# Kernel optimization log

Hardware: AMD Instinct MI355X
Metric: run time of the kernel (lower is better)

Reference implementation:

```python
import jax, jax.numpy as jnp
import numpy as np
from jax import lax

B, T, N_MELS = 8, 4096, 26
W_FRAMES = 32          # window_frames
CONV_CH, CONV_K = 64, 5
SE_MID = CONV_CH // 4  # se_ratio=4 on feature_dim=conv_channels
H1, H2 = 256, 128      # hidden_dims
SHORT_W, SHORT_H = 8, 128
OUT_CH = 2             # downbeat=True


def setup_inputs() -> dict:
    key = jax.random.key(0)
    ks = jax.random.split(key, 16)
    s = lambda *sh: 1.0 / np.sqrt(sh[0])
    return {
        "x": jax.random.normal(ks[0], (B, T, N_MELS), jnp.float32),
        # conv1d: kernel stored (K, in, out) for NWC/WIO conv
        "conv_w": jax.random.normal(ks[1], (CONV_K, N_MELS, CONV_CH), jnp.float32) * 0.1,
        "conv_b": jax.random.normal(ks[2], (CONV_CH,), jnp.float32) * 0.1,
        # SE on feature_dim=CONV_CH
        "se_w1": jax.random.normal(ks[3], (CONV_CH, SE_MID), jnp.float32) * s(CONV_CH),
        "se_b1": jnp.zeros((SE_MID,), jnp.float32),
        "se_w2": jax.random.normal(ks[4], (SE_MID, CONV_CH), jnp.float32) * s(SE_MID),
        "se_b2": jnp.zeros((CONV_CH,), jnp.float32),
        # long backbone: (W_FRAMES*CONV_CH) -> H1 -> H2
        "w1": jax.random.normal(ks[5], (W_FRAMES * CONV_CH, H1), jnp.float32) * s(W_FRAMES * CONV_CH),
        "b1": jnp.zeros((H1,), jnp.float32),
        "w2": jax.random.normal(ks[6], (H1, H2), jnp.float32) * s(H1),
        "b2": jnp.zeros((H2,), jnp.float32),
        # short backbone: (SHORT_W*CONV_CH) -> SHORT_H
        "sw": jax.random.normal(ks[7], (SHORT_W * CONV_CH, SHORT_H), jnp.float32) * s(SHORT_W * CONV_CH),
        "sb": jnp.zeros((SHORT_H,), jnp.float32),
        # output head: (H2 + SHORT_H) -> OUT_CH
        "wo": jax.random.normal(ks[8], (H2 + SHORT_H, OUT_CH), jnp.float32) * s(H2 + SHORT_H),
        "bo": jnp.zeros((OUT_CH,), jnp.float32),
    }


def reference(x, conv_w, conv_b, se_w1, se_b1, se_w2, se_b2,
              w1, b1, w2, b2, sw, sb, wo, bo):
    batch, time, _ = x.shape
    # 1) causal conv1d over full sequence (left-pad K-1), then ReLU
    xp = jnp.pad(x, ((0, 0), (CONV_K - 1, 0), (0, 0)))
    xc = lax.conv_general_dilated(xp, conv_w, window_strides=(1,),
                                  padding='VALID',
                                  dimension_numbers=('NWC', 'WIO', 'NWC'))
    xc = jax.nn.relu(xc + conv_b)                      # (B, T, F=CONV_CH)
    # 2) causal sliding-window unfold: windows[b,t,w,:] = padded[b, t+w, :]
    x_pad = jnp.pad(xc, ((0, 0), (W_FRAMES - 1, 0), (0, 0)))
    idx = jnp.arange(time)[:, None] + jnp.arange(W_FRAMES)[None, :]
    windows = x_pad[:, idx, :]                          # (B, T, W, F)
    # 3) SE channel attention (pool over window dim)
    s = windows.mean(axis=2)                            # (B, T, F)
    a = jax.nn.sigmoid(jax.nn.relu(s @ se_w1 + se_b1) @ se_w2 + se_b2)
    windows = windows * a[:, :, None, :]
    # 4) long backbone (dropout = identity in eval)
    flat_long = windows.reshape(batch, time, W_FRAMES * CONV_CH)
    h = jax.nn.relu(flat_long @ w1 + b1)
    h = jax.nn.relu(h @ w2 + b2)                        # (B, T, H2)
    # short path: last SHORT_W frames of the same SE-processed window
    flat_short = windows[:, :, -SHORT_W:, :].reshape(batch, time, SHORT_W * CONV_CH)
    h_short = jax.nn.relu(flat_short @ sw + sb)         # (B, T, SHORT_H)
    h = jnp.concatenate([h, h_short], axis=-1)
    # 5) output head
    return jax.nn.sigmoid(h @ wo + bo)                  # (B, T, OUT_CH)
```

## Files before the change

### kernel.cpp

```cpp
#include <hip/hip_runtime.h>

typedef _Float16 half_t;
typedef __attribute__((ext_vector_type(8))) _Float16 h8;
typedef __attribute__((ext_vector_type(2))) _Float16 h2v;
typedef __attribute__((ext_vector_type(4))) float f4;
typedef __attribute__((ext_vector_type(2))) float f2v;

__device__ __forceinline__ half_t to_h(float v) {
    v = fminf(fmaxf(v, -60000.f), 60000.f);
    return (half_t)v;
}

__global__ void pack_k(const float* __restrict__ w1, const float* __restrict__ w2,
                       const float* __restrict__ sw, const float* __restrict__ cw,
                       half_t* __restrict__ wsH) {
    int i = blockIdx.x * 256 + threadIdx.x;
    if (i < 65536) {
        int L = i & 63, nt = (i >> 6) & 15, kk = i >> 10;
        int k0 = kk * 32 + ((L >> 4) << 3), n = (nt << 4) + (L & 15);
        h8 v;
#pragma unroll
        for (int j = 0; j < 8; j++) v[j] = to_h(w1[(k0 + j) * 256 + n]);
        *(h8*)(wsH + ((((kk * 16 + nt) * 64 + L)) << 3)) = v;
    } else if (i < 69632) {
        int o = i - 65536;
        int L = o & 63, nt = (o >> 6) & 7, kk = o >> 9;
        int k0 = kk * 32 + ((L >> 4) << 3), n = (nt << 4) + (L & 15);
        h8 v;
#pragma unroll
        for (int j = 0; j < 8; j++) v[j] = to_h(w2[(k0 + j) * 128 + n]);
        *(h8*)(wsH + 524288 + ((((kk * 8 + nt) * 64 + L)) << 3)) = v;
    } else if (i < 77824) {
        int o = i - 69632;
        int L = o & 63, nt = (o >> 6) & 7, kk = o >> 9;
        int k0 = kk * 32 + ((L >> 4) << 3), n = (nt << 4) + (L & 15);
        h8 v;
#pragma unroll
        for (int j = 0; j < 8; j++) v[j] = to_h(sw[(k0 + j) * 128 + n]);
        *(h8*)(wsH + 557056 + ((((kk * 8 + nt) * 64 + L)) << 3)) = v;
    } else if (i < 86144) {
        int o = i - 77824;
        int c = o & 63, rest = o >> 6;
        int k = rest / 26, ci = rest - k * 26;
        int ip = ci >> 1, r = ci & 1;
        wsH[622592 + ((k * 13 + ip) * 64 + c) * 2 + r] = to_h(cw[o]);
    }
}

#define XCS 72
#define ALS 72
#define Y1S 264
#define SLS 68
#define HLS 20

#define MFMA16(a, b, c) __builtin_amdgcn_mfma_f32_16x16x32_f16(a, b, c, 0, 0, 0)

__global__ __launch_bounds__(512, 4) void beat_main(
    const float* __restrict__ x,
    const float* __restrict__ conv_b,
    const float* __restrict__ se_w1, const float* __restrict__ se_b1,
    const float* __restrict__ se_w2, const float* __restrict__ se_b2,
    const float* __restrict__ b1, const float* __restrict__ b2,
    const float* __restrict__ sb,
    const float* __restrict__ wo, const float* __restrict__ bo,
    const half_t* __restrict__ w1p, const half_t* __restrict__ w2p,
    const half_t* __restrict__ swp, const half_t* __restrict__ cwp,
    float* __restrict__ out) {

    __shared__ __align__(16) char smem[58752];
    half_t* xcL = (half_t*)smem;
    half_t* aL  = (half_t*)(smem + 13696);
    char*   U   = smem + 22912;
    half_t* xLh = (half_t*)U;
    float*  sLf = (float*)U;
    float*  hidL= (float*)(U + 17408);
    half_t* y1L = (half_t*)U;
    float*  woL = (float*)(smem + 56704);

    const int tid = threadIdx.x;
    const int bi = blockIdx.x;
    const int b = bi >> 6;
    const int t0 = (bi & 63) << 6;
    const int lane = tid & 63, wv = tid >> 6;
    const int quad = lane >> 4, rl = lane & 15;

    if (tid < 256) ((f2v*)woL)[tid] = ((const f2v*)wo)[tid];
    for (int idx = tid; idx < 99 * 13; idx += 512) {
        int fi = idx / 13, ip = idx - fi * 13;
        int tx = t0 - 35 + fi;
        h2v v;
        if (tx >= 0) {
            const float* xp = x + ((size_t)(b * 4096 + tx)) * 26 + 2 * ip;
            v[0] = to_h(xp[0]); v[1] = to_h(xp[1]);
        } else { v[0] = (_Float16)0.f; v[1] = (_Float16)0.f; }
        *(h2v*)(xLh + fi * 28 + 2 * ip) = v;
    }
    __syncthreads();

    {
        int c = tid & 63, f0 = tid >> 6;
        h2v cwr[65];
        const h2v* cwg = (const h2v*)cwp;
#pragma unroll
        for (int p = 0; p < 65; p++) cwr[p] = cwg[p * 64 + c];
        float bias = conv_b[c];
        for (int f = f0; f < 95; f += 8) {
            int t = t0 - 31 + f;
            float r0 = 0.f;
            if (t >= 0) {
                h2v accp; accp[0] = (_Float16)0.f; accp[1] = (_Float16)0.f;
#pragma unroll
                for (int k = 0; k < 5; k++)
#pragma unroll
                    for (int ip = 0; ip < 13; ip++) {
                        h2v xp = *(const h2v*)(xLh + (f + k) * 28 + 2 * ip);
                        accp += xp * cwr[k * 13 + ip];
                    }
                r0 = fmaxf((float)accp[0] + (float)accp[1] + bias, 0.f);
            }
            xcL[f * XCS + c] = to_h(r0);
        }
    }
    __syncthreads();

    {
        int c = tid & 63, mb = tid >> 6;
        float run = 0.f;
#pragma unroll 8
        for (int w = 0; w < 32; w++) run += (float)xcL[(mb + w) * XCS + c];
        sLf[mb * SLS + c] = run * (1.f / 32.f);
        for (int m = mb + 8; m < 64; m += 8) {
#pragma unroll
            for (int d = 0; d < 8; d++) {
                run += (float)xcL[(m + 24 + d) * XCS + c];
                run -= (float)xcL[(m - 8 + d) * XCS + c];
            }
            sLf[m * SLS + c] = run * (1.f / 32.f);
        }
    }
    __syncthreads();

    {
        int m = tid >> 3, hh = (tid & 7) * 2;
        float acc0 = se_b1[hh], acc1 = se_b1[hh + 1];
        for (int c = 0; c < 64; c++) {
            float sv = sLf[m * SLS + c];
            f2v wq = *(const f2v*)(se_w1 + c * 16 + hh);
            acc0 += sv * wq[0]; acc1 += sv * wq[1];
        }
        hidL[m * HLS + hh] = fmaxf(acc0, 0.f);
        hidL[m * HLS + hh + 1] = fmaxf(acc1, 0.f);
    }
    __syncthreads();

    {
        int m = tid >> 3, c0 = (tid & 7) * 8;
        float av[8];
#pragma unroll
        for (int j = 0; j < 8; j++) av[j] = se_b2[c0 + j];
        for (int h = 0; h < 16; h++) {
            float hv = hidL[m * HLS + h];
            const f4* wv4 = (const f4*)(se_w2 + h * 64 + c0);
            f4 wq0 = wv4[0], wq1 = wv4[1];
#pragma unroll
            for (int j = 0; j < 4; j++) { av[j] += hv * wq0[j]; av[4 + j] += hv * wq1[j]; }
        }
#pragma unroll
        for (int j = 0; j < 8; j++) {
            float zz = fminf(fmaxf(av[j], -30.f), 30.f);
            float s = 1.f / (1.f + __expf(-zz));
            aL[m * ALS + c0 + j] = to_h(s);
        }
    }
    __syncthreads();

    h8 avr[4][2];
#pragma unroll
    for (int mt = 0; mt < 4; mt++)
#pragma unroll
        for (int p = 0; p < 2; p++)
            avr[mt][p] = *(const h8*)(aL + (mt * 16 + rl) * ALS + p * 32 + quad * 8);

    {
        f4 acc[4][2];
#pragma unroll
        for (int mt = 0; mt < 4; mt++)
#pragma unroll
            for (int i = 0; i < 2; i++)
#pragma unroll
                for (int r = 0; r < 4; r++) acc[mt][i][r] = 0.f;
        const h8* w1v = (const h8*)w1p;
        const int fb = wv * 2;
        h8 bA[2], bB[2], bC[2], bD[2];
#pragma unroll
        for (int i = 0; i < 2; i++) bA[i] = w1v[(fb + i) * 64 + lane];
#pragma unroll
        for (int i = 0; i < 2; i++) bB[i] = w1v[(16 + fb + i) * 64 + lane];
#pragma unroll 2
        for (int kk = 0; kk < 64; kk += 2) {
            const int k2 = (kk + 2) & 63, k3 = (kk + 3) & 63;
#pragma unroll
            for (int i = 0; i < 2; i++) bC[i] = w1v[(k2 * 16 + fb + i) * 64 + lane];
#pragma unroll
            for (int i = 0; i < 2; i++) bD[i] = w1v[(k3 * 16 + fb + i) * 64 + lane];
            const int wf = kk >> 1;
            {
                const int c0 = quad * 8;
#pragma unroll
                for (int mt = 0; mt < 4; mt++) {
                    int m = mt * 16 + rl;
                    h8 xv = *(const h8*)(xcL + (m + wf) * XCS + c0);
                    h8 af = xv * avr[mt][0];
                    acc[mt][0] = MFMA16(af, bA[0], acc[mt][0]);
                    acc[mt][1] = MFMA16(af, bA[1], acc[mt][1]);
                }
            }
            {
                const int c0 = 32 + quad * 8;
#pragma unroll
                for (int mt = 0; mt < 4; mt++) {
                    int m = mt * 16 + rl;
                    h8 xv = *(const h8*)(xcL + (m + wf) * XCS + c0);
                    h8 af = xv * avr[mt][1];
                    acc[mt][0] = MFMA16(af, bB[0], acc[mt][0]);
                    acc[mt][1] = MFMA16(af, bB[1], acc[mt][1]);
                }
            }
#pragma unroll
            for (int i = 0; i < 2; i++) { bA[i] = bC[i]; bB[i] = bD[i]; }
        }
#pragma unroll
        for (int i = 0; i < 2; i++) {
            int n = wv * 32 + i * 16 + rl;
            float bb = b1[n];
#pragma unroll
            for (int mt = 0; mt < 4; mt++)
#pragma unroll
                for (int r = 0; r < 4; r++) {
                    int m = mt * 16 + quad * 4 + r;
                    y1L[m * Y1S + n] = to_h(fmaxf(acc[mt][i][r] + bb, 0.f));
                }
        }
    }
    __syncthreads();

    f4 acc2[4];
#pragma unroll
    for (int mt = 0; mt < 4; mt++)
#pragma unroll
        for (int r = 0; r < 4; r++) acc2[mt][r] = 0.f;
    {
        const h8* w2v = (const h8*)w2p;
        h8 cf = w2v[wv * 64 + lane];
#pragma unroll 2
        for (int kk = 0; kk < 8; kk++) {
            int kn = (kk + 1) & 7;
            h8 nf = w2v[(kn * 8 + wv) * 64 + lane];
#pragma unroll
            for (int mt = 0; mt < 4; mt++) {
                h8 av = *(const h8*)(y1L + (mt * 16 + rl) * Y1S + kk * 32 + quad * 8);
                acc2[mt] = MFMA16(av, cf, acc2[mt]);
            }
            cf = nf;
        }
    }

    f4 accS[4];
#pragma unroll
    for (int mt = 0; mt < 4; mt++)
#pragma unroll
        for (int r = 0; r < 4; r++) accS[mt][r] = 0.f;
    {
        const h8* swv = (const h8*)swp;
        h8 cf = swv[wv * 64 + lane];
#pragma unroll 2
        for (int kk = 0; kk < 16; kk++) {
            int kn = (kk + 1) & 15;
            h8 nf = swv[(kn * 8 + wv) * 64 + lane];
            const int wf = 24 + (kk >> 1);
            const int c0 = ((kk & 1) << 5) + quad * 8;
#pragma unroll
            for (int mt = 0; mt < 4; mt++) {
                int m = mt * 16 + rl;
                h8 xv = *(const h8*)(xcL + (m + wf) * XCS + c0);
                h8 af = xv * avr[mt][kk & 1];
                accS[mt] = MFMA16(af, cf, accS[mt]);
            }
            cf = nf;
        }
    }
    __syncthreads();

    {
        int n = wv * 16 + rl;
        float bb2 = b2[n], bbs = sb[n];
#pragma unroll
        for (int mt = 0; mt < 4; mt++)
#pragma unroll
            for (int r = 0; r < 4; r++) {
                int m = mt * 16 + quad * 4 + r;
                y1L[m * Y1S + n]       = to_h(fmaxf(acc2[mt][r] + bb2, 0.f));
                y1L[m * Y1S + 128 + n] = to_h(fmaxf(accS[mt][r] + bbs, 0.f));
            }
    }
    __syncthreads();

    if (tid < 128) {
        int m = tid >> 1, o = tid & 1;
        float z = bo[o];
        const half_t* hrow = y1L + m * Y1S;
        for (int nb = 0; nb < 32; nb++) {
            h8 hv = *(const h8*)(hrow + nb * 8);
#pragma unroll
            for (int q = 0; q < 8; q++)
                z += (float)hv[q] * woL[(nb * 8 + q) * 2 + o];
        }
        z = fminf(fmaxf(z, -30.f), 30.f);
        float sg = 1.f / (1.f + __expf(-z));
        out[((size_t)(b * 4096 + t0 + m)) * 2 + o] = sg;
    }
}

extern "C" void kernel_launch(void* const* d_in, const int* in_sizes, int n_in,
                              void* d_out, int out_size, void* d_ws, size_t ws_size,
                              hipStream_t stream) {
    const float* x      = (const float*)d_in[0];
    const float* conv_w = (const float*)d_in[1];
    const float* conv_b = (const float*)d_in[2];
    const float* se_w1  = (const float*)d_in[3];
    const float* se_b1  = (const float*)d_in[4];
    const float* se_w2  = (const float*)d_in[5];
    const float* se_b2  = (const float*)d_in[6];
    const float* w1     = (const float*)d_in[7];
    const float* b1     = (const float*)d_in[8];
    const float* w2     = (const float*)d_in[9];
    const float* b2     = (const float*)d_in[10];
    const float* sw     = (const float*)d_in[11];
    const float* sb     = (const float*)d_in[12];
    const float* wo     = (const float*)d_in[13];
    const float* bo     = (const float*)d_in[14];
    half_t* wsH = (half_t*)d_ws;

    hipLaunchKernelGGL(pack_k, dim3(337), dim3(256), 0, stream, w1, w2, sw, conv_w, wsH);
    hipLaunchKernelGGL(beat_main, dim3(512), dim3(512), 0, stream,
                       x, conv_b, se_w1, se_b1, se_w2, se_b2, b1, b2, sb, wo, bo,
                       wsH, wsH + 524288, wsH + 557056, wsH + 622592,
                       (float*)d_out);
}
```

Before: 147.5 us.

## Shrink LDS footprint, interleave W2/short GEMMs, split output head across all threads

Reorganizes shared memory so y1L overlays the SE attention buffer, which shrinks the allocation and may allow more resident blocks per CU. An extra barrier is added after the attention values are copied into registers. The conv accumulation is split into two fp16 accumulators to shorten the dependency chain. The W2 and short-path MFMA loops are interleaved, and the xcL loads in the W1 loop are batched ahead of the MFMAs. The output head now runs on all 512 threads with partial sums reduced through LDS, at the cost of an extra barrier.

```diff
diff --git a/kernel.cpp b/kernel.cpp
--- a/kernel.cpp
+++ b/kernel.cpp
@@ -67,15 +67,15 @@
     const half_t* __restrict__ swp, const half_t* __restrict__ cwp,
     float* __restrict__ out) {
 
-    __shared__ __align__(16) char smem[58752];
+    __shared__ __align__(16) char smem[49536];
     half_t* xcL = (half_t*)smem;
     half_t* aL  = (half_t*)(smem + 13696);
-    char*   U   = smem + 22912;
-    half_t* xLh = (half_t*)U;
-    float*  sLf = (float*)U;
-    float*  hidL= (float*)(U + 17408);
-    half_t* y1L = (half_t*)U;
-    float*  woL = (float*)(smem + 56704);
+    half_t* y1L = (half_t*)(smem + 13696);
+    half_t* xLh = (half_t*)(smem + 22912);
+    float*  sLf = (float*)(smem + 22912);
+    float*  hidL= (float*)(smem + 40320);
+    float*  woL = (float*)(smem + 47488);
+    float*  redL= (float*)smem;
 
     const int tid = threadIdx.x;
     const int bi = blockIdx.x;
@@ -108,15 +108,17 @@
             int t = t0 - 31 + f;
             float r0 = 0.f;
             if (t >= 0) {
-                h2v accp; accp[0] = (_Float16)0.f; accp[1] = (_Float16)0.f;
+                h2v a0; a0[0] = (_Float16)0.f; a0[1] = (_Float16)0.f;
+                h2v a1 = a0;
 #pragma unroll
                 for (int k = 0; k < 5; k++)
 #pragma unroll
                     for (int ip = 0; ip < 13; ip++) {
+                        int p = k * 13 + ip;
                         h2v xp = *(const h2v*)(xLh + (f + k) * 28 + 2 * ip);
-                        accp += xp * cwr[k * 13 + ip];
+                        if (p & 1) a1 += xp * cwr[p]; else a0 += xp * cwr[p];
                     }
-                r0 = fmaxf((float)accp[0] + (float)accp[1] + bias, 0.f);
+                r0 = fmaxf((float)a0[0] + (float)a0[1] + (float)a1[0] + (float)a1[1] + bias, 0.f);
             }
             xcL[f * XCS + c] = to_h(r0);
         }
@@ -180,6 +182,7 @@
 #pragma unroll
         for (int p = 0; p < 2; p++)
             avr[mt][p] = *(const h8*)(aL + (mt * 16 + rl) * ALS + p * 32 + quad * 8);
+    __syncthreads();
 
     {
         f4 acc[4][2];
@@ -206,22 +209,26 @@
             const int wf = kk >> 1;
             {
                 const int c0 = quad * 8;
+                h8 xv[4];
+#pragma unroll
+                for (int mt = 0; mt < 4; mt++)
+                    xv[mt] = *(const h8*)(xcL + (mt * 16 + rl + wf) * XCS + c0);
 #pragma unroll
                 for (int mt = 0; mt < 4; mt++) {
-                    int m = mt * 16 + rl;
-                    h8 xv = *(const h8*)(xcL + (m + wf) * XCS + c0);
-                    h8 af = xv * avr[mt][0];
+                    h8 af = xv[mt] * avr[mt][0];
                     acc[mt][0] = MFMA16(af, bA[0], acc[mt][0]);
                     acc[mt][1] = MFMA16(af, bA[1], acc[mt][1]);
                 }
             }
             {
                 const int c0 = 32 + quad * 8;
+                h8 xv[4];
+#pragma unroll
+                for (int mt = 0; mt < 4; mt++)
+                    xv[mt] = *(const h8*)(xcL + (mt * 16 + rl + wf) * XCS + c0);
 #pragma unroll
                 for (int mt = 0; mt < 4; mt++) {
-                    int m = mt * 16 + rl;
-                    h8 xv = *(const h8*)(xcL + (m + wf) * XCS + c0);
-                    h8 af = xv * avr[mt][1];
+                    h8 af = xv[mt] * avr[mt][1];
                     acc[mt][0] = MFMA16(af, bB[0], acc[mt][0]);
                     acc[mt][1] = MFMA16(af, bB[1], acc[mt][1]);
                 }
@@ -244,49 +251,44 @@
     }
     __syncthreads();
 
-    f4 acc2[4];
+    f4 acc2[4], accS[4];
 #pragma unroll
     for (int mt = 0; mt < 4; mt++)
 #pragma unroll
-        for (int r = 0; r < 4; r++) acc2[mt][r] = 0.f;
+        for (int r = 0; r < 4; r++) { acc2[mt][r] = 0.f; accS[mt][r] = 0.f; }
     {
         const h8* w2v = (const h8*)w2p;
-        h8 cf = w2v[wv * 64 + lane];
+        const h8* swv = (const h8*)swp;
+        h8 c2 = w2v[wv * 64 + lane];
+        h8 cs = swv[wv * 64 + lane];
 #pragma unroll 2
         for (int kk = 0; kk < 8; kk++) {
-            int kn = (kk + 1) & 7;
-            h8 nf = w2v[(kn * 8 + wv) * 64 + lane];
-#pragma unroll
-            for (int mt = 0; mt < 4; mt++) {
-                h8 av = *(const h8*)(y1L + (mt * 16 + rl) * Y1S + kk * 32 + quad * 8);
-                acc2[mt] = MFMA16(av, cf, acc2[mt]);
-            }
-            cf = nf;
-        }
-    }
-
-    f4 accS[4];
-#pragma unroll
-    for (int mt = 0; mt < 4; mt++)
-#pragma unroll
-        for (int r = 0; r < 4; r++) accS[mt][r] = 0.f;
-    {
-        const h8* swv = (const h8*)swp;
-        h8 cf = swv[wv * 64 + lane];
-#pragma unroll 2
-        for (int kk = 0; kk < 16; kk++) {
-            int kn = (kk + 1) & 15;
-            h8 nf = swv[(kn * 8 + wv) * 64 + lane];
+            h8 ns = swv[(((kk + 1) & 15) * 8 + wv) * 64 + lane];
+            h8 n2 = w2v[(((kk + 1) & 7) * 8 + wv) * 64 + lane];
             const int wf = 24 + (kk >> 1);
             const int c0 = ((kk & 1) << 5) + quad * 8;
 #pragma unroll
             for (int mt = 0; mt < 4; mt++) {
-                int m = mt * 16 + rl;
-                h8 xv = *(const h8*)(xcL + (m + wf) * XCS + c0);
+                h8 xv = *(const h8*)(xcL + (mt * 16 + rl + wf) * XCS + c0);
                 h8 af = xv * avr[mt][kk & 1];
-                accS[mt] = MFMA16(af, cf, accS[mt]);
-            }
-            cf = nf;
+                accS[mt] = MFMA16(af, cs, accS[mt]);
+                h8 av = *(const h8*)(y1L + (mt * 16 + rl) * Y1S + kk * 32 + quad * 8);
+                acc2[mt] = MFMA16(av, c2, acc2[mt]);
+            }
+            cs = ns; c2 = n2;
+        }
+#pragma unroll 2
+        for (int kk = 8; kk < 16; kk++) {
+            h8 ns = swv[(((kk + 1) & 15) * 8 + wv) * 64 + lane];
+            const int wf = 24 + (kk >> 1);
+            const int c0 = ((kk & 1) << 5) + quad * 8;
+#pragma unroll
+            for (int mt = 0; mt < 4; mt++) {
+                h8 xv = *(const h8*)(xcL + (mt * 16 + rl + wf) * XCS + c0);
+                h8 af = xv * avr[mt][kk & 1];
+                accS[mt] = MFMA16(af, cs, accS[mt]);
+            }
+            cs = ns;
         }
     }
     __syncthreads();
@@ -305,16 +307,23 @@
     }
     __syncthreads();
 
+    {
+        int o = tid & 1, c4 = (tid >> 1) & 3, m = tid >> 3;
+        float part = 0.f;
+        const half_t* hrow = y1L + m * Y1S + c4 * 64;
+        for (int nb = 0; nb < 8; nb++) {
+            h8 hv = *(const h8*)(hrow + nb * 8);
+#pragma unroll
+            for (int q = 0; q < 8; q++)
+                part += (float)hv[q] * woL[(c4 * 64 + nb * 8 + q) * 2 + o];
+        }
+        redL[tid] = part;
+    }
+    __syncthreads();
     if (tid < 128) {
         int m = tid >> 1, o = tid & 1;
-        float z = bo[o];
-        const half_t* hrow = y1L + m * Y1S;
-        for (int nb = 0; nb < 32; nb++) {
-            h8 hv = *(const h8*)(hrow + nb * 8);
-#pragma unroll
-            for (int q = 0; q < 8; q++)
-                z += (float)hv[q] * woL[(nb * 8 + q) * 2 + o];
-        }
+        float z = bo[o] + redL[m * 8 + o] + redL[m * 8 + 2 + o]
+                        + redL[m * 8 + 4 + o] + redL[m * 8 + 6 + o];
         z = fminf(fmaxf(z, -30.f), 30.f);
         float sg = 1.f / (1.f + __expf(-z));
         out[((size_t)(b * 4096 + t0 + m)) * 2 + o] = sg;
```

Result: slower. 158.3 us (+7.4%).

## Switch GEMMs to 32x32x16 MFMA with repacked weights and tighter LDS strides

Applied to the files above, without the earlier changes.

Replaces the 16x16x32 MFMA tiling with 32x32x16 MFMA for the long, second-layer and short GEMMs. The weight packing is redone to match the 32-wide B-fragment layout, and the LDS row strides shrink from 72 to 68 halves. The wave-to-tile mapping also changes, so each wave now owns a 32x32 output tile in the second layer and the short path. The goal is fewer LDS A-fragment reloads per FLOP and less instruction overhead. The risks are different LDS bank-conflict behaviour with the new stride and longer MFMA dependency chains on only two accumulators.

```diff
diff --git a/kernel.cpp b/kernel.cpp
--- a/kernel.cpp
+++ b/kernel.cpp
@@ -4,6 +4,7 @@
 typedef __attribute__((ext_vector_type(8))) _Float16 h8;
 typedef __attribute__((ext_vector_type(2))) _Float16 h2v;
 typedef __attribute__((ext_vector_type(4))) float f4;
+typedef __attribute__((ext_vector_type(16))) float f16v;
 typedef __attribute__((ext_vector_type(2))) float f2v;
 
 __device__ __forceinline__ half_t to_h(float v) {
@@ -16,28 +17,28 @@
                        half_t* __restrict__ wsH) {
     int i = blockIdx.x * 256 + threadIdx.x;
     if (i < 65536) {
-        int L = i & 63, nt = (i >> 6) & 15, kk = i >> 10;
-        int k0 = kk * 32 + ((L >> 4) << 3), n = (nt << 4) + (L & 15);
+        int L = i & 63, nt = (i >> 6) & 7, ks = i >> 9;
+        int k0 = ks * 16 + ((L >> 5) << 3), n = nt * 32 + (L & 31);
         h8 v;
 #pragma unroll
         for (int j = 0; j < 8; j++) v[j] = to_h(w1[(k0 + j) * 256 + n]);
-        *(h8*)(wsH + ((((kk * 16 + nt) * 64 + L)) << 3)) = v;
+        *(h8*)(wsH + ((size_t)i << 3)) = v;
     } else if (i < 69632) {
         int o = i - 65536;
-        int L = o & 63, nt = (o >> 6) & 7, kk = o >> 9;
-        int k0 = kk * 32 + ((L >> 4) << 3), n = (nt << 4) + (L & 15);
+        int L = o & 63, nt = (o >> 6) & 3, ks = o >> 8;
+        int k0 = ks * 16 + ((L >> 5) << 3), n = nt * 32 + (L & 31);
         h8 v;
 #pragma unroll
         for (int j = 0; j < 8; j++) v[j] = to_h(w2[(k0 + j) * 128 + n]);
-        *(h8*)(wsH + 524288 + ((((kk * 8 + nt) * 64 + L)) << 3)) = v;
+        *(h8*)(wsH + 524288 + ((size_t)o << 3)) = v;
     } else if (i < 77824) {
         int o = i - 69632;
-        int L = o & 63, nt = (o >> 6) & 7, kk = o >> 9;
-        int k0 = kk * 32 + ((L >> 4) << 3), n = (nt << 4) + (L & 15);
+        int L = o & 63, nt = (o >> 6) & 3, ks = o >> 8;
+        int k0 = ks * 16 + ((L >> 5) << 3), n = nt * 32 + (L & 31);
         h8 v;
 #pragma unroll
         for (int j = 0; j < 8; j++) v[j] = to_h(sw[(k0 + j) * 128 + n]);
-        *(h8*)(wsH + 557056 + ((((kk * 8 + nt) * 64 + L)) << 3)) = v;
+        *(h8*)(wsH + 557056 + ((size_t)o << 3)) = v;
     } else if (i < 86144) {
         int o = i - 77824;
         int c = o & 63, rest = o >> 6;
@@ -47,13 +48,13 @@
     }
 }
 
-#define XCS 72
-#define ALS 72
+#define XCS 68
+#define ALS 68
 #define Y1S 264
 #define SLS 68
 #define HLS 20
 
-#define MFMA16(a, b, c) __builtin_amdgcn_mfma_f32_16x16x32_f16(a, b, c, 0, 0, 0)
+#define MFMA32(a, b, c) __builtin_amdgcn_mfma_f32_32x32x16_f16(a, b, c, 0, 0, 0)
 
 __global__ __launch_bounds__(512, 4) void beat_main(
     const float* __restrict__ x,
@@ -67,22 +68,22 @@
     const half_t* __restrict__ swp, const half_t* __restrict__ cwp,
     float* __restrict__ out) {
 
-    __shared__ __align__(16) char smem[58752];
+    __shared__ __align__(16) char smem[57472];
     half_t* xcL = (half_t*)smem;
-    half_t* aL  = (half_t*)(smem + 13696);
-    char*   U   = smem + 22912;
+    half_t* aL  = (half_t*)(smem + 12928);
+    char*   U   = smem + 21632;
     half_t* xLh = (half_t*)U;
     float*  sLf = (float*)U;
-    float*  hidL= (float*)(U + 17408);
+    float*  hidL= (float*)(smem + 39040);
     half_t* y1L = (half_t*)U;
-    float*  woL = (float*)(smem + 56704);
+    float*  woL = (float*)(smem + 55424);
 
     const int tid = threadIdx.x;
     const int bi = blockIdx.x;
     const int b = bi >> 6;
     const int t0 = (bi & 63) << 6;
     const int lane = tid & 63, wv = tid >> 6;
-    const int quad = lane >> 4, rl = lane & 15;
+    const int l31 = lane & 31, khalf = lane >> 5;
 
     if (tid < 256) ((f2v*)woL)[tid] = ((const f2v*)wo)[tid];
     for (int idx = tid; idx < 99 * 13; idx += 512) {
@@ -174,134 +175,107 @@
     }
     __syncthreads();
 
-    h8 avr[4][2];
-#pragma unroll
-    for (int mt = 0; mt < 4; mt++)
-#pragma unroll
-        for (int p = 0; p < 2; p++)
-            avr[mt][p] = *(const h8*)(aL + (mt * 16 + rl) * ALS + p * 32 + quad * 8);
-
-    {
-        f4 acc[4][2];
-#pragma unroll
-        for (int mt = 0; mt < 4; mt++)
-#pragma unroll
-            for (int i = 0; i < 2; i++)
-#pragma unroll
-                for (int r = 0; r < 4; r++) acc[mt][i][r] = 0.f;
-        const h8* w1v = (const h8*)w1p;
-        const int fb = wv * 2;
-        h8 bA[2], bB[2], bC[2], bD[2];
-#pragma unroll
-        for (int i = 0; i < 2; i++) bA[i] = w1v[(fb + i) * 64 + lane];
-#pragma unroll
-        for (int i = 0; i < 2; i++) bB[i] = w1v[(16 + fb + i) * 64 + lane];
+    {
+        f16v acc0, acc1;
+#pragma unroll
+        for (int r = 0; r < 16; r++) { acc0[r] = 0.f; acc1[r] = 0.f; }
+        h8 avr[2][4];
+#pragma unroll
+        for (int m32 = 0; m32 < 2; m32++)
+#pragma unroll
+            for (int s = 0; s < 4; s++)
+                avr[m32][s] = *(const h8*)(aL + (m32 * 32 + l31) * ALS + s * 16 + khalf * 8);
+        const h8* bp = ((const h8*)w1p) + wv * 64 + lane;
+        h8 bP0 = bp[0], bP1 = bp[512];
+        const half_t* xr0 = xcL + l31 * XCS + khalf * 8;
+        const half_t* xr1 = xcL + (32 + l31) * XCS + khalf * 8;
+        for (int q = 0; q < 32; q++) {
+            h8 bN0 = bp[(q * 4 + 2) * 512];
+            {
+                h8 x0 = *(const h8*)(xr0), x1 = *(const h8*)(xr1);
+                acc0 = MFMA32(x0 * avr[0][0], bP0, acc0);
+                acc1 = MFMA32(x1 * avr[1][0], bP0, acc1);
+            }
+            h8 bN1 = bp[(q * 4 + 3) * 512];
+            {
+                h8 x0 = *(const h8*)(xr0 + 16), x1 = *(const h8*)(xr1 + 16);
+                acc0 = MFMA32(x0 * avr[0][1], bP1, acc0);
+                acc1 = MFMA32(x1 * avr[1][1], bP1, acc1);
+            }
+            bP0 = bp[((q * 4 + 4) & 127) * 512];
+            {
+                h8 x0 = *(const h8*)(xr0 + 32), x1 = *(const h8*)(xr1 + 32);
+                acc0 = MFMA32(x0 * avr[0][2], bN0, acc0);
+                acc1 = MFMA32(x1 * avr[1][2], bN0, acc1);
+            }
+            bP1 = bp[((q * 4 + 5) & 127) * 512];
+            {
+                h8 x0 = *(const h8*)(xr0 + 48), x1 = *(const h8*)(xr1 + 48);
+                acc0 = MFMA32(x0 * avr[0][3], bN1, acc0);
+                acc1 = MFMA32(x1 * avr[1][3], bN1, acc1);
+            }
+            xr0 += XCS; xr1 += XCS;
+        }
+        int n = wv * 32 + l31;
+        float bb = b1[n];
+#pragma unroll
+        for (int r = 0; r < 16; r++) {
+            int row = (r & 3) + 8 * (r >> 2) + 4 * khalf;
+            y1L[row * Y1S + n]        = to_h(fmaxf(acc0[r] + bb, 0.f));
+            y1L[(32 + row) * Y1S + n] = to_h(fmaxf(acc1[r] + bb, 0.f));
+        }
+    }
+    __syncthreads();
+
+    f16v acc2;
+#pragma unroll
+    for (int r = 0; r < 16; r++) acc2[r] = 0.f;
+    {
+        const int m32 = wv >> 2, nt = wv & 3;
+        const h8* bp2 = ((const h8*)w2p) + nt * 64 + lane;
+        const half_t* ar = y1L + (m32 * 32 + l31) * Y1S + khalf * 8;
+        h8 bc = bp2[0];
 #pragma unroll 2
-        for (int kk = 0; kk < 64; kk += 2) {
-            const int k2 = (kk + 2) & 63, k3 = (kk + 3) & 63;
-#pragma unroll
-            for (int i = 0; i < 2; i++) bC[i] = w1v[(k2 * 16 + fb + i) * 64 + lane];
-#pragma unroll
-            for (int i = 0; i < 2; i++) bD[i] = w1v[(k3 * 16 + fb + i) * 64 + lane];
-            const int wf = kk >> 1;
-            {
-                const int c0 = quad * 8;
-#pragma unroll
-                for (int mt = 0; mt < 4; mt++) {
-                    int m = mt * 16 + rl;
-                    h8 xv = *(const h8*)(xcL + (m + wf) * XCS + c0);
-                    h8 af = xv * avr[mt][0];
-                    acc[mt][0] = MFMA16(af, bA[0], acc[mt][0]);
-                    acc[mt][1] = MFMA16(af, bA[1], acc[mt][1]);
-                }
-            }
-            {
-                const int c0 = 32 + quad * 8;
-#pragma unroll
-                for (int mt = 0; mt < 4; mt++) {
-                    int m = mt * 16 + rl;
-                    h8 xv = *(const h8*)(xcL + (m + wf) * XCS + c0);
-                    h8 af = xv * avr[mt][1];
-                    acc[mt][0] = MFMA16(af, bB[0], acc[mt][0]);
-                    acc[mt][1] = MFMA16(af, bB[1], acc[mt][1]);
-                }
-            }
-#pragma unroll
-            for (int i = 0; i < 2; i++) { bA[i] = bC[i]; bB[i] = bD[i]; }
-        }
-#pragma unroll
-        for (int i = 0; i < 2; i++) {
-            int n = wv * 32 + i * 16 + rl;
-            float bb = b1[n];
-#pragma unroll
-            for (int mt = 0; mt < 4; mt++)
-#pragma unroll
-                for (int r = 0; r < 4; r++) {
-                    int m = mt * 16 + quad * 4 + r;
-                    y1L[m * Y1S + n] = to_h(fmaxf(acc[mt][i][r] + bb, 0.f));
-                }
-        }
-    }
-    __syncthreads();
-
-    f4 acc2[4];
-#pragma unroll
-    for (int mt = 0; mt < 4; mt++)
-#pragma unroll
-        for (int r = 0; r < 4; r++) acc2[mt][r] = 0.f;
-    {
-        const h8* w2v = (const h8*)w2p;
-        h8 cf = w2v[wv * 64 + lane];
+        for (int ks = 0; ks < 16; ks++) {
+            h8 bn = bp2[((ks + 1) & 15) * 256];
+            h8 av = *(const h8*)(ar + ks * 16);
+            acc2 = MFMA32(av, bc, acc2);
+            bc = bn;
+        }
+    }
+
+    f16v accS;
+#pragma unroll
+    for (int r = 0; r < 16; r++) accS[r] = 0.f;
+    {
+        const int m32 = wv >> 2, nt = wv & 3;
+        const h8* bps = ((const h8*)swp) + nt * 64 + lane;
+        const half_t* arow = aL + (m32 * 32 + l31) * ALS + khalf * 8;
+        const half_t* xrow = xcL + (m32 * 32 + l31) * XCS + khalf * 8;
+        h8 bc = bps[0];
 #pragma unroll 2
-        for (int kk = 0; kk < 8; kk++) {
-            int kn = (kk + 1) & 7;
-            h8 nf = w2v[(kn * 8 + wv) * 64 + lane];
-#pragma unroll
-            for (int mt = 0; mt < 4; mt++) {
-                h8 av = *(const h8*)(y1L + (mt * 16 + rl) * Y1S + kk * 32 + quad * 8);
-                acc2[mt] = MFMA16(av, cf, acc2[mt]);
-            }
-            cf = nf;
-        }
-    }
-
-    f4 accS[4];
-#pragma unroll
-    for (int mt = 0; mt < 4; mt++)
-#pragma unroll
-        for (int r = 0; r < 4; r++) accS[mt][r] = 0.f;
-    {
-        const h8* swv = (const h8*)swp;
-        h8 cf = swv[wv * 64 + lane];
-#pragma unroll 2
-        for (int kk = 0; kk < 16; kk++) {
-            int kn = (kk + 1) & 15;
-            h8 nf = swv[(kn * 8 + wv) * 64 + lane];
-            const int wf = 24 + (kk >> 1);
-            const int c0 = ((kk & 1) << 5) + quad * 8;
-#pragma unroll
-            for (int mt = 0; mt < 4; mt++) {
-                int m = mt * 16 + rl;
-                h8 xv = *(const h8*)(xcL + (m + wf) * XCS + c0);
-                h8 af = xv * avr[mt][kk & 1];
-                accS[mt] = MFMA16(af, cf, accS[mt]);
-            }
-            cf = nf;
-        }
-    }
-    __syncthreads();
-
-    {
-        int n = wv * 16 + rl;
+        for (int ks = 0; ks < 32; ks++) {
+            h8 bn = bps[((ks + 1) & 31) * 256];
+            const int wf = 24 + (ks >> 2);
+            const int c0 = (ks & 3) * 16;
+            h8 xv = *(const h8*)(xrow + wf * XCS + c0);
+            h8 gv = *(const h8*)(arow + c0);
+            accS = MFMA32(xv * gv, bc, accS);
+            bc = bn;
+        }
+    }
+    __syncthreads();
+
+    {
+        const int m32 = wv >> 2, nt = wv & 3;
+        int n = nt * 32 + l31;
         float bb2 = b2[n], bbs = sb[n];
 #pragma unroll
-        for (int mt = 0; mt < 4; mt++)
-#pragma unroll
-            for (int r = 0; r < 4; r++) {
-                int m = mt * 16 + quad * 4 + r;
-                y1L[m * Y1S + n]       = to_h(fmaxf(acc2[mt][r] + bb2, 0.f));
-                y1L[m * Y1S + 128 + n] = to_h(fmaxf(accS[mt][r] + bbs, 0.f));
-            }
+        for (int r = 0; r < 16; r++) {
+            int m = m32 * 32 + (r & 3) + 8 * (r >> 2) + 4 * khalf;
+            y1L[m * Y1S + n]       = to_h(fmaxf(acc2[r] + bb2, 0.f));
+            y1L[m * Y1S + 128 + n] = to_h(fmaxf(accS[r] + bbs, 0.f));
+        }
     }
     __syncthreads();
 
```

After: 253.4 us. 1.72x slower.
